# Optimization experiments

Measured on AMD Instinct MI355X. Metric: run time of the kernel, lower is better.

Reference implementation:

```python
import jax, jax.numpy as jnp
import numpy as np

N_NODES = 100000
N_EDGES = 1600000
D_IN = 128
D_OUT = 128


def setup_inputs() -> dict:
    key = jax.random.key(0)
    k = jax.random.split(key, 6)
    x = jax.random.normal(k[0], (N_NODES, D_IN), dtype=jnp.float32)
    edge_src = jax.random.randint(k[1], (N_EDGES,), 0, N_NODES, dtype=jnp.int64)
    edge_dst = jax.random.randint(k[2], (N_EDGES,), 0, N_NODES, dtype=jnp.int64)
    edge_weight = jax.random.uniform(k[3], (N_EDGES,), dtype=jnp.float32)
    # xavier-uniform-ish init for the two projection matrices
    lim = float(np.sqrt(6.0 / (D_IN + D_OUT)))
    W_nbrs = jax.random.uniform(k[4], (D_IN, D_OUT), minval=-lim, maxval=lim, dtype=jnp.float32)
    W_self = jax.random.uniform(k[5], (D_IN, D_OUT), minval=-lim, maxval=lim, dtype=jnp.float32)
    bias = jnp.zeros((D_OUT,), dtype=jnp.float32)
    return {"x": x, "edge_src": edge_src, "edge_dst": edge_dst,
            "edge_weight": edge_weight, "W_nbrs": W_nbrs, "W_self": W_self,
            "bias": bias}


def reference(x, edge_src, edge_dst, edge_weight, W_nbrs, W_self, bias):
    # y = x @ W_nbrs  (dense projection)
    y = x @ W_nbrs                                   # [N, D_OUT]
    # spmm(adj, y): out[i] = sum_{(j->i) in E} w_ij * y[j]
    msgs = edge_weight[:, None] * y[edge_src]        # [E, D_OUT]
    agg = jax.ops.segment_sum(msgs, edge_dst, num_segments=x.shape[0])
    # self transform + bias
    return agg + x @ W_self + bias
```

## Files before the change

kernel.cpp:

```cpp
#include <hip/hip_runtime.h>
#include <hip/hip_bf16.h>

#define D 128

typedef __bf16 bf16x8 __attribute__((ext_vector_type(8)));
typedef unsigned short u16x8 __attribute__((ext_vector_type(8)));
typedef float f32x4 __attribute__((ext_vector_type(4)));

__device__ __forceinline__ unsigned short f2bf(float f) {
    unsigned u = __float_as_uint(f);
    u += 0x7FFFu + ((u >> 16) & 1u);
    return (unsigned short)(u >> 16);
}
__device__ __forceinline__ float bf2f(unsigned u16) {
    return __uint_as_float(u16 << 16);
}

__global__ void k_build_wt(const float* __restrict__ Wn, const float* __restrict__ Ws,
                           unsigned short* __restrict__ WTs,
                           int* __restrict__ cnt, int N) {
    int g = blockIdx.x * blockDim.x + threadIdx.x;
    int c = g >> 7;
    int k = g & 127;
    float v = (c < 128) ? Wn[k * 128 + c] : Ws[k * 128 + (c - 128)];
    WTs[c * 128 + k] = f2bf(v);
    for (int i = g; i < N; i += 32768) cnt[i] = 0;
}

__global__ __launch_bounds__(256) void k_gemm_rank(
    const float* __restrict__ x, const unsigned short* __restrict__ WTs,
    const float* __restrict__ bias, int N,
    unsigned short* __restrict__ y, float* __restrict__ out,
    const int* __restrict__ edst, int E,
    int* __restrict__ cnt, int* __restrict__ rank) {
    int b = blockIdx.x;
    int tid = threadIdx.x;
    if (b & 1) {
        int e0 = (b >> 1) * 1024 + tid;
        #pragma unroll
        for (int k = 0; k < 4; ++k) {
            int e = e0 + k * 256;
            if (e < E) rank[e] = atomicAdd(&cnt[edst[e]], 1);
        }
        return;
    }
    int gb = b >> 1;
    int brow = gb * 64;
    if (brow >= N) return;
    int w = tid >> 6, l = tid & 63;
    int row0 = brow + w * 16;
    int c15 = l & 15;
    int kgrp = l >> 4;
    int arow = row0 + c15;
    bool avalid = (arow < N);
    const float* xr = x + (size_t)arow * D;
    bf16x8 afrag[4];
    #pragma unroll
    for (int ks = 0; ks < 4; ++ks) {
        int k0 = ks * 32 + kgrp * 8;
        float4 a0, a1;
        if (avalid) { a0 = *(const float4*)(xr + k0); a1 = *(const float4*)(xr + k0 + 4); }
        else { a0 = make_float4(0.f, 0.f, 0.f, 0.f); a1 = a0; }
        bf16x8 f;
        f[0] = (__bf16)a0.x; f[1] = (__bf16)a0.y; f[2] = (__bf16)a0.z; f[3] = (__bf16)a0.w;
        f[4] = (__bf16)a1.x; f[5] = (__bf16)a1.y; f[6] = (__bf16)a1.z; f[7] = (__bf16)a1.w;
        afrag[ks] = f;
    }
    int orow = row0 + kgrp * 4;
    const unsigned short* Bbase = WTs + (size_t)c15 * 128 + kgrp * 8;
    f32x4 acc[8];
    #pragma unroll
    for (int nt = 0; nt < 8; ++nt) {
        f32x4 a = {0.f, 0.f, 0.f, 0.f};
        #pragma unroll
        for (int ks = 0; ks < 4; ++ks) {
            const bf16x8* bp = (const bf16x8*)(Bbase + nt * 16 * 128 + ks * 32);
            a = __builtin_amdgcn_mfma_f32_16x16x32_bf16(afrag[ks], *bp, a, 0, 0, 0);
        }
        acc[nt] = a;
    }
    #pragma unroll
    for (int j = 0; j < 4; ++j) {
        int r = orow + j;
        if (r < N) {
            u16x8 f;
            #pragma unroll
            for (int nt = 0; nt < 8; ++nt) f[nt] = f2bf(acc[nt][j]);
            *(u16x8*)(y + (size_t)r * D + c15 * 8) = f;
        }
    }
    #pragma unroll
    for (int nt = 0; nt < 8; ++nt) {
        f32x4 a = {0.f, 0.f, 0.f, 0.f};
        #pragma unroll
        for (int ks = 0; ks < 4; ++ks) {
            const bf16x8* bp = (const bf16x8*)(Bbase + (128 + nt * 16) * 128 + ks * 32);
            a = __builtin_amdgcn_mfma_f32_16x16x32_bf16(afrag[ks], *bp, a, 0, 0, 0);
        }
        acc[nt] = a;
    }
    float bv[8];
    #pragma unroll
    for (int nt = 0; nt < 8; ++nt) bv[nt] = bias[nt * 16 + c15];
    #pragma unroll
    for (int j = 0; j < 4; ++j) {
        int r = orow + j;
        if (r < N) {
            float4 s0 = make_float4(acc[0][j] + bv[0], acc[1][j] + bv[1],
                                    acc[2][j] + bv[2], acc[3][j] + bv[3]);
            float4 s1 = make_float4(acc[4][j] + bv[4], acc[5][j] + bv[5],
                                    acc[6][j] + bv[6], acc[7][j] + bv[7]);
            float4* op = (float4*)(out + (size_t)r * D + c15 * 8);
            op[0] = s0; op[1] = s1;
        }
    }
}

__global__ void k_scanA(const int* __restrict__ cnt, int N,
                        int* __restrict__ ofs, int* __restrict__ bsum) {
    __shared__ int lds[1024];
    int t = threadIdx.x, i = blockIdx.x * 1024 + t;
    int v = (i < N) ? cnt[i] : 0;
    lds[t] = v; __syncthreads();
    for (int d = 1; d < 1024; d <<= 1) {
        int x = (t >= d) ? lds[t - d] : 0; __syncthreads();
        lds[t] += x; __syncthreads();
    }
    if (i < N) ofs[i] = lds[t] - v;
    if (t == 1023) bsum[blockIdx.x] = lds[t];
}

__global__ void k_scanB(int* __restrict__ bsum, int NB) {
    __shared__ int lds[128];
    int t = threadIdx.x;
    int v = (t < NB) ? bsum[t] : 0;
    lds[t] = v; __syncthreads();
    for (int d = 1; d < 128; d <<= 1) {
        int x = (t >= d) ? lds[t - d] : 0; __syncthreads();
        lds[t] += x; __syncthreads();
    }
    if (t < NB) bsum[t] = lds[t] - v;
}

__global__ __launch_bounds__(256) void k_fill(
    const int* __restrict__ src, const int* __restrict__ dst,
    const float* __restrict__ w, const int* __restrict__ rank, int E,
    const int* __restrict__ ofs, const int* __restrict__ bsum,
    uint2* __restrict__ sorted) {
    int e0 = blockIdx.x * 1024 + threadIdx.x;
    #pragma unroll
    for (int k = 0; k < 4; ++k) {
        int e = e0 + k * 256;
        if (e < E) {
            int d = dst[e];
            int pos = ofs[d] + bsum[d >> 10] + rank[e];
            sorted[pos] = make_uint2((unsigned)src[e], __float_as_uint(w[e]));
        }
    }
}

__global__ __launch_bounds__(256) void k_agg(
    const unsigned short* __restrict__ y, const uint2* __restrict__ sorted,
    const int* __restrict__ ofs, const int* __restrict__ bsum,
    const int* __restrict__ cnt, int N,
    float* __restrict__ out) {
    int w = threadIdx.x >> 6, l = threadIdx.x & 63;
    int node = blockIdx.x * 4 + w;
    if (node >= N) return;
    int s = ofs[node] + bsum[node >> 10], n = cnt[node];
    int g = l >> 4, li = l & 15;
    float4 s0, s1;
    if (l < 16) {
        const float4* spf = (const float4*)(out + (size_t)node * D + li * 8);
        s0 = spf[0]; s1 = spf[1];
    }
    const uint2* sp = sorted + s;
    float a0 = 0.f, a1 = 0.f, a2 = 0.f, a3 = 0.f;
    float a4 = 0.f, a5 = 0.f, a6 = 0.f, a7 = 0.f;
    int j = g;
    for (; j + 4 < n; j += 8) {
        uint2 pa = sp[j];
        uint2 pb = sp[j + 4];
        uint4 va = *(const uint4*)(y + (size_t)pa.x * D + li * 8);
        uint4 vb = *(const uint4*)(y + (size_t)pb.x * D + li * 8);
        float wa = __uint_as_float(pa.y), wb = __uint_as_float(pb.y);
        a0 += wa * bf2f(va.x & 0xFFFFu); a1 += wa * bf2f(va.x >> 16);
        a2 += wa * bf2f(va.y & 0xFFFFu); a3 += wa * bf2f(va.y >> 16);
        a4 += wa * bf2f(va.z & 0xFFFFu); a5 += wa * bf2f(va.z >> 16);
        a6 += wa * bf2f(va.w & 0xFFFFu); a7 += wa * bf2f(va.w >> 16);
        a0 += wb * bf2f(vb.x & 0xFFFFu); a1 += wb * bf2f(vb.x >> 16);
        a2 += wb * bf2f(vb.y & 0xFFFFu); a3 += wb * bf2f(vb.y >> 16);
        a4 += wb * bf2f(vb.z & 0xFFFFu); a5 += wb * bf2f(vb.z >> 16);
        a6 += wb * bf2f(vb.w & 0xFFFFu); a7 += wb * bf2f(vb.w >> 16);
    }
    if (j < n) {
        uint2 p = sp[j];
        uint4 v = *(const uint4*)(y + (size_t)p.x * D + li * 8);
        float wt = __uint_as_float(p.y);
        a0 += wt * bf2f(v.x & 0xFFFFu); a1 += wt * bf2f(v.x >> 16);
        a2 += wt * bf2f(v.y & 0xFFFFu); a3 += wt * bf2f(v.y >> 16);
        a4 += wt * bf2f(v.z & 0xFFFFu); a5 += wt * bf2f(v.z >> 16);
        a6 += wt * bf2f(v.w & 0xFFFFu); a7 += wt * bf2f(v.w >> 16);
    }
    a0 += __shfl_xor(a0, 16, 64); a1 += __shfl_xor(a1, 16, 64);
    a2 += __shfl_xor(a2, 16, 64); a3 += __shfl_xor(a3, 16, 64);
    a4 += __shfl_xor(a4, 16, 64); a5 += __shfl_xor(a5, 16, 64);
    a6 += __shfl_xor(a6, 16, 64); a7 += __shfl_xor(a7, 16, 64);
    a0 += __shfl_xor(a0, 32, 64); a1 += __shfl_xor(a1, 32, 64);
    a2 += __shfl_xor(a2, 32, 64); a3 += __shfl_xor(a3, 32, 64);
    a4 += __shfl_xor(a4, 32, 64); a5 += __shfl_xor(a5, 32, 64);
    a6 += __shfl_xor(a6, 32, 64); a7 += __shfl_xor(a7, 32, 64);
    if (l < 16) {
        float* op = out + (size_t)node * D + li;
        op[0]   = a0 + s0.x; op[16]  = a1 + s0.y;
        op[32]  = a2 + s0.z; op[48]  = a3 + s0.w;
        op[64]  = a4 + s1.x; op[80]  = a5 + s1.y;
        op[96]  = a6 + s1.z; op[112] = a7 + s1.w;
    }
}

extern "C" void kernel_launch(void* const* d_in, const int* in_sizes, int n_in,
                              void* d_out, int out_size, void* d_ws, size_t ws_size,
                              hipStream_t stream) {
    const float* x    = (const float*)d_in[0];
    const int*   esrc = (const int*)d_in[1];
    const int*   edst = (const int*)d_in[2];
    const float* ew   = (const float*)d_in[3];
    const float* Wn   = (const float*)d_in[4];
    const float* Wsf  = (const float*)d_in[5];
    const float* bias = (const float*)d_in[6];
    float* out = (float*)d_out;
    int N = in_sizes[0] / D;
    int E = in_sizes[1];

    char* ws = (char*)d_ws;
    size_t off = 0;
    unsigned short* WTs = (unsigned short*)(ws + off); off += 256 * 128 * sizeof(unsigned short);
    unsigned short* yb  = (unsigned short*)(ws + off); off += (size_t)N * D * sizeof(unsigned short);
    off = (off + 255) & ~(size_t)255;
    int* cnt  = (int*)(ws + off); off += (size_t)N * 4; off = (off + 255) & ~(size_t)255;
    int* ofs  = (int*)(ws + off); off += (size_t)N * 4; off = (off + 255) & ~(size_t)255;
    int* bsum = (int*)(ws + off); off += 1024;
    int* rank = (int*)(ws + off); off += (size_t)E * 4; off = (off + 255) & ~(size_t)255;
    uint2* sorted = (uint2*)(ws + off); off += (size_t)E * 8;

    k_build_wt<<<128, 256, 0, stream>>>(Wn, Wsf, WTs, cnt, N);

    int GB = (N + 63) / 64;
    int RB = (E + 1023) / 1024;
    int G2 = (GB > RB ? GB : RB) * 2;
    k_gemm_rank<<<G2, 256, 0, stream>>>(x, WTs, bias, N, yb, out,
                                        edst, E, cnt, rank);

    int NB = (N + 1023) / 1024;
    k_scanA<<<NB, 1024, 0, stream>>>(cnt, N, ofs, bsum);
    k_scanB<<<1, 128, 0, stream>>>(bsum, NB);
    k_fill<<<(E + 1023) / 1024, 256, 0, stream>>>(esrc, edst, ew, rank, E, ofs, bsum, sorted);

    k_agg<<<(N + 3) / 4, 256, 0, stream>>>(yb, sorted, ofs, bsum, cnt, N, out);
}
```

Before: 352.0 us.

## Stage swizzled weight tiles in LDS and double GEMM rows per block

Weights are now written in an XOR-swizzled transposed layout and staged into 32KB of shared memory per GEMM block, one matrix at a time, instead of being read from global/L2 for every MFMA. Each GEMM block now covers 128 rows (two 16-row tiles per wave), so each weight load is reused across more rows. The block interleave is changed to one GEMM block per two rank blocks to match. This cuts repeated global weight traffic but adds LDS usage that lowers occupancy, plus extra barriers.

Result: faster. 300.6 us (-14.6%).

```diff
diff --git a/kernel.cpp b/kernel.cpp
--- a/kernel.cpp
+++ b/kernel.cpp
@@ -20,10 +20,11 @@
                            unsigned short* __restrict__ WTs,
                            int* __restrict__ cnt, int N) {
     int g = blockIdx.x * blockDim.x + threadIdx.x;
-    int c = g >> 7;
-    int k = g & 127;
+    int k = g >> 8;
+    int c = g & 255;
     float v = (c < 128) ? Wn[k * 128 + c] : Ws[k * 128 + (c - 128)];
-    WTs[c * 128 + k] = f2bf(v);
+    int chunk = k >> 3;
+    WTs[c * 128 + (((chunk ^ (c & 15)) << 3) | (k & 7))] = f2bf(v);
     for (int i = g; i < N; i += 32768) cnt[i] = 0;
 }
 
@@ -33,10 +34,12 @@
     unsigned short* __restrict__ y, float* __restrict__ out,
     const int* __restrict__ edst, int E,
     int* __restrict__ cnt, int* __restrict__ rank) {
+    __shared__ unsigned short sm[128 * 128];
     int b = blockIdx.x;
     int tid = threadIdx.x;
-    if (b & 1) {
-        int e0 = (b >> 1) * 1024 + tid;
+    if (b % 3 != 0) {
+        int rb = (b / 3) * 2 + (b % 3) - 1;
+        int e0 = rb * 1024 + tid;
         #pragma unroll
         for (int k = 0; k < 4; ++k) {
             int e = e0 + k * 256;
@@ -44,74 +47,102 @@
         }
         return;
     }
-    int gb = b >> 1;
-    int brow = gb * 64;
+    int gb = b / 3;
+    int brow = gb * 128;
     if (brow >= N) return;
     int w = tid >> 6, l = tid & 63;
-    int row0 = brow + w * 16;
+    int row0 = brow + w * 32;
     int c15 = l & 15;
     int kgrp = l >> 4;
-    int arow = row0 + c15;
-    bool avalid = (arow < N);
-    const float* xr = x + (size_t)arow * D;
-    bf16x8 afrag[4];
-    #pragma unroll
-    for (int ks = 0; ks < 4; ++ks) {
-        int k0 = ks * 32 + kgrp * 8;
-        float4 a0, a1;
-        if (avalid) { a0 = *(const float4*)(xr + k0); a1 = *(const float4*)(xr + k0 + 4); }
-        else { a0 = make_float4(0.f, 0.f, 0.f, 0.f); a1 = a0; }
-        bf16x8 f;
-        f[0] = (__bf16)a0.x; f[1] = (__bf16)a0.y; f[2] = (__bf16)a0.z; f[3] = (__bf16)a0.w;
-        f[4] = (__bf16)a1.x; f[5] = (__bf16)a1.y; f[6] = (__bf16)a1.z; f[7] = (__bf16)a1.w;
-        afrag[ks] = f;
-    }
-    int orow = row0 + kgrp * 4;
-    const unsigned short* Bbase = WTs + (size_t)c15 * 128 + kgrp * 8;
-    f32x4 acc[8];
-    #pragma unroll
-    for (int nt = 0; nt < 8; ++nt) {
-        f32x4 a = {0.f, 0.f, 0.f, 0.f};
+    const uint4* gs = (const uint4*)WTs;
+    uint4* ss = (uint4*)sm;
+    uint4 st[8];
+    #pragma unroll
+    for (int r = 0; r < 8; ++r) st[r] = gs[r * 256 + tid];
+    bf16x8 afrag[2][4];
+    #pragma unroll
+    for (int rt = 0; rt < 2; ++rt) {
+        int arow = row0 + rt * 16 + c15;
+        bool avalid = (arow < N);
+        const float* xr = x + (size_t)arow * D;
         #pragma unroll
         for (int ks = 0; ks < 4; ++ks) {
-            const bf16x8* bp = (const bf16x8*)(Bbase + nt * 16 * 128 + ks * 32);
-            a = __builtin_amdgcn_mfma_f32_16x16x32_bf16(afrag[ks], *bp, a, 0, 0, 0);
-        }
-        acc[nt] = a;
-    }
-    #pragma unroll
-    for (int j = 0; j < 4; ++j) {
-        int r = orow + j;
-        if (r < N) {
-            u16x8 f;
+            int k0 = ks * 32 + kgrp * 8;
+            float4 a0, a1;
+            if (avalid) { a0 = *(const float4*)(xr + k0); a1 = *(const float4*)(xr + k0 + 4); }
+            else { a0 = make_float4(0.f, 0.f, 0.f, 0.f); a1 = a0; }
+            bf16x8 f;
+            f[0] = (__bf16)a0.x; f[1] = (__bf16)a0.y; f[2] = (__bf16)a0.z; f[3] = (__bf16)a0.w;
+            f[4] = (__bf16)a1.x; f[5] = (__bf16)a1.y; f[6] = (__bf16)a1.z; f[7] = (__bf16)a1.w;
+            afrag[rt][ks] = f;
+        }
+    }
+    #pragma unroll
+    for (int r = 0; r < 8; ++r) ss[r * 256 + tid] = st[r];
+    __syncthreads();
+    #pragma unroll
+    for (int rt = 0; rt < 2; ++rt) {
+        f32x4 acc[8];
+        #pragma unroll
+        for (int nt = 0; nt < 8; ++nt) {
+            int c = nt * 16 + c15;
+            f32x4 a = {0.f, 0.f, 0.f, 0.f};
             #pragma unroll
-            for (int nt = 0; nt < 8; ++nt) f[nt] = f2bf(acc[nt][j]);
-            *(u16x8*)(y + (size_t)r * D + c15 * 8) = f;
-        }
-    }
-    #pragma unroll
-    for (int nt = 0; nt < 8; ++nt) {
-        f32x4 a = {0.f, 0.f, 0.f, 0.f};
-        #pragma unroll
-        for (int ks = 0; ks < 4; ++ks) {
-            const bf16x8* bp = (const bf16x8*)(Bbase + (128 + nt * 16) * 128 + ks * 32);
-            a = __builtin_amdgcn_mfma_f32_16x16x32_bf16(afrag[ks], *bp, a, 0, 0, 0);
-        }
-        acc[nt] = a;
-    }
+            for (int ks = 0; ks < 4; ++ks) {
+                int chunk = ks * 4 + kgrp;
+                const bf16x8* bp = (const bf16x8*)(sm + c * 128 + ((chunk ^ c15) << 3));
+                a = __builtin_amdgcn_mfma_f32_16x16x32_bf16(afrag[rt][ks], *bp, a, 0, 0, 0);
+            }
+            acc[nt] = a;
+        }
+        int orow = row0 + rt * 16 + kgrp * 4;
+        #pragma unroll
+        for (int j = 0; j < 4; ++j) {
+            int r = orow + j;
+            if (r < N) {
+                u16x8 f;
+                #pragma unroll
+                for (int nt = 0; nt < 8; ++nt) f[nt] = f2bf(acc[nt][j]);
+                *(u16x8*)(y + (size_t)r * D + c15 * 8) = f;
+            }
+        }
+    }
+    __syncthreads();
+    #pragma unroll
+    for (int r = 0; r < 8; ++r) st[r] = gs[2048 + r * 256 + tid];
+    #pragma unroll
+    for (int r = 0; r < 8; ++r) ss[r * 256 + tid] = st[r];
+    __syncthreads();
     float bv[8];
     #pragma unroll
     for (int nt = 0; nt < 8; ++nt) bv[nt] = bias[nt * 16 + c15];
     #pragma unroll
-    for (int j = 0; j < 4; ++j) {
-        int r = orow + j;
-        if (r < N) {
-            float4 s0 = make_float4(acc[0][j] + bv[0], acc[1][j] + bv[1],
-                                    acc[2][j] + bv[2], acc[3][j] + bv[3]);
-            float4 s1 = make_float4(acc[4][j] + bv[4], acc[5][j] + bv[5],
-                                    acc[6][j] + bv[6], acc[7][j] + bv[7]);
-            float4* op = (float4*)(out + (size_t)r * D + c15 * 8);
-            op[0] = s0; op[1] = s1;
+    for (int rt = 0; rt < 2; ++rt) {
+        f32x4 acc[8];
+        #pragma unroll
+        for (int nt = 0; nt < 8; ++nt) {
+            int c = nt * 16 + c15;
+            f32x4 a = {0.f, 0.f, 0.f, 0.f};
+            #pragma unroll
+            for (int ks = 0; ks < 4; ++ks) {
+                int chunk = ks * 4 + kgrp;
+                const bf16x8* bp = (const bf16x8*)(sm + c * 128 + ((chunk ^ c15) << 3));
+                a = __builtin_amdgcn_mfma_f32_16x16x32_bf16(afrag[rt][ks], *bp, a, 0, 0, 0);
+            }
+            acc[nt] = a;
+        }
+        int orow = row0 + rt * 16 + kgrp * 4;
+        #pragma unroll
+        for (int j = 0; j < 4; ++j) {
+            int r = orow + j;
+            if (r < N) {
+                float4 s0 = make_float4(acc[0][j] + bv[0], acc[1][j] + bv[1],
+                                        acc[2][j] + bv[2], acc[3][j] + bv[3]);
+                float4 s1 = make_float4(acc[4][j] + bv[4], acc[5][j] + bv[5],
+                                        acc[6][j] + bv[6], acc[7][j] + bv[7]);
+                float4* op = (float4*)(out + (size_t)r * D + c15 * 8);
+                op[0] = s0; op[1] = s1;
+            }
         }
     }
 }
@@ -246,11 +277,12 @@
 
     k_build_wt<<<128, 256, 0, stream>>>(Wn, Wsf, WTs, cnt, N);
 
-    int GB = (N + 63) / 64;
+    int GB = (N + 127) / 128;
     int RB = (E + 1023) / 1024;
-    int G2 = (GB > RB ? GB : RB) * 2;
-    k_gemm_rank<<<G2, 256, 0, stream>>>(x, WTs, bias, N, yb, out,
-                                        edst, E, cnt, rank);
+    int RBH = (RB + 1) / 2;
+    int M = (GB > RBH ? GB : RBH);
+    k_gemm_rank<<<M * 3, 256, 0, stream>>>(x, WTs, bias, N, yb, out,
+                                           edst, E, cnt, rank);
 
     int NB = (N + 1023) / 1024;
     k_scanA<<<NB, 1024, 0, stream>>>(cnt, N, ofs, bsum);
```

## Split GEMM across rank and fill phases, stage weights in swizzled LDS

Applied to the files above, without the earlier changes.

Splits the fused GEMM into two kernels. The neighbour projection runs alongside the edge-rank atomics, and the self projection plus bias runs alongside the sorted-edge fill, which replaces the standalone fill kernel. Each GEMM block now stages its 128x128 bf16 weight half in LDS using an XOR-swizzled layout written by the weight-build kernel, and the rank and fill paths use vectorized int4 loads. This aims to balance work between the two phases and cut repeated global weight reads, at the cost of reading x twice and using 32KB of LDS per block, which can reduce occupancy.

New measurement: 296.6 us. -15.7%, faster.

```diff
diff --git a/kernel.cpp b/kernel.cpp
--- a/kernel.cpp
+++ b/kernel.cpp
@@ -20,27 +20,34 @@
                            unsigned short* __restrict__ WTs,
                            int* __restrict__ cnt, int N) {
     int g = blockIdx.x * blockDim.x + threadIdx.x;
-    int c = g >> 7;
-    int k = g & 127;
+    int k = g >> 8;
+    int c = g & 255;
     float v = (c < 128) ? Wn[k * 128 + c] : Ws[k * 128 + (c - 128)];
-    WTs[c * 128 + k] = f2bf(v);
+    int chunk = k >> 3;
+    WTs[c * 128 + (((chunk ^ (c & 15)) << 3) | (k & 7))] = f2bf(v);
     for (int i = g; i < N; i += 32768) cnt[i] = 0;
 }
 
-__global__ __launch_bounds__(256) void k_gemm_rank(
-    const float* __restrict__ x, const unsigned short* __restrict__ WTs,
-    const float* __restrict__ bias, int N,
-    unsigned short* __restrict__ y, float* __restrict__ out,
+__global__ __launch_bounds__(256) void k1_gemm_y_rank(
+    const float* __restrict__ x, const unsigned short* __restrict__ WTs, int N,
+    unsigned short* __restrict__ y,
     const int* __restrict__ edst, int E,
     int* __restrict__ cnt, int* __restrict__ rank) {
+    __shared__ unsigned short sm[128 * 128];
     int b = blockIdx.x;
     int tid = threadIdx.x;
     if (b & 1) {
-        int e0 = (b >> 1) * 1024 + tid;
-        #pragma unroll
-        for (int k = 0; k < 4; ++k) {
-            int e = e0 + k * 256;
-            if (e < E) rank[e] = atomicAdd(&cnt[edst[e]], 1);
+        int e0 = (b >> 1) * 1024 + tid * 4;
+        if (e0 + 3 < E) {
+            int4 d4 = *(const int4*)(edst + e0);
+            int r0 = atomicAdd(&cnt[d4.x], 1);
+            int r1 = atomicAdd(&cnt[d4.y], 1);
+            int r2 = atomicAdd(&cnt[d4.z], 1);
+            int r3 = atomicAdd(&cnt[d4.w], 1);
+            *(int4*)(rank + e0) = make_int4(r0, r1, r2, r3);
+        } else {
+            for (int e = e0; e < E && e < e0 + 4; ++e)
+                rank[e] = atomicAdd(&cnt[edst[e]], 1);
         }
         return;
     }
@@ -51,6 +58,11 @@
     int row0 = brow + w * 16;
     int c15 = l & 15;
     int kgrp = l >> 4;
+    const uint4* gs = (const uint4*)WTs;
+    uint4* ss = (uint4*)sm;
+    uint4 st[8];
+    #pragma unroll
+    for (int r = 0; r < 8; ++r) st[r] = gs[r * 256 + tid];
     int arow = row0 + c15;
     bool avalid = (arow < N);
     const float* xr = x + (size_t)arow * D;
@@ -66,19 +78,23 @@
         f[4] = (__bf16)a1.x; f[5] = (__bf16)a1.y; f[6] = (__bf16)a1.z; f[7] = (__bf16)a1.w;
         afrag[ks] = f;
     }
-    int orow = row0 + kgrp * 4;
-    const unsigned short* Bbase = WTs + (size_t)c15 * 128 + kgrp * 8;
+    #pragma unroll
+    for (int r = 0; r < 8; ++r) ss[r * 256 + tid] = st[r];
+    __syncthreads();
     f32x4 acc[8];
     #pragma unroll
     for (int nt = 0; nt < 8; ++nt) {
+        int c = nt * 16 + c15;
         f32x4 a = {0.f, 0.f, 0.f, 0.f};
         #pragma unroll
         for (int ks = 0; ks < 4; ++ks) {
-            const bf16x8* bp = (const bf16x8*)(Bbase + nt * 16 * 128 + ks * 32);
+            int chunk = ks * 4 + kgrp;
+            const bf16x8* bp = (const bf16x8*)(sm + c * 128 + ((chunk ^ c15) << 3));
             a = __builtin_amdgcn_mfma_f32_16x16x32_bf16(afrag[ks], *bp, a, 0, 0, 0);
         }
         acc[nt] = a;
     }
+    int orow = row0 + kgrp * 4;
     #pragma unroll
     for (int j = 0; j < 4; ++j) {
         int r = orow + j;
@@ -89,12 +105,104 @@
             *(u16x8*)(y + (size_t)r * D + c15 * 8) = f;
         }
     }
+}
+
+__global__ void k_scanA(const int* __restrict__ cnt, int N,
+                        int* __restrict__ ofs, int* __restrict__ bsum) {
+    __shared__ int lds[1024];
+    int t = threadIdx.x, i = blockIdx.x * 1024 + t;
+    int v = (i < N) ? cnt[i] : 0;
+    lds[t] = v; __syncthreads();
+    for (int d = 1; d < 1024; d <<= 1) {
+        int x = (t >= d) ? lds[t - d] : 0; __syncthreads();
+        lds[t] += x; __syncthreads();
+    }
+    if (i < N) ofs[i] = lds[t] - v;
+    if (t == 1023) bsum[blockIdx.x] = lds[t];
+}
+
+__global__ void k_scanB(int* __restrict__ bsum, int NB) {
+    __shared__ int lds[128];
+    int t = threadIdx.x;
+    int v = (t < NB) ? bsum[t] : 0;
+    lds[t] = v; __syncthreads();
+    for (int d = 1; d < 128; d <<= 1) {
+        int x = (t >= d) ? lds[t - d] : 0; __syncthreads();
+        lds[t] += x; __syncthreads();
+    }
+    if (t < NB) bsum[t] = lds[t] - v;
+}
+
+__global__ __launch_bounds__(256) void k2_gemm_self_fill(
+    const float* __restrict__ x, const unsigned short* __restrict__ WTs,
+    const float* __restrict__ bias, int N,
+    float* __restrict__ out,
+    const int* __restrict__ src, const int* __restrict__ dst,
+    const float* __restrict__ ew, const int* __restrict__ rank, int E,
+    const int* __restrict__ ofs, const int* __restrict__ bsum,
+    uint2* __restrict__ sorted) {
+    __shared__ unsigned short sm[128 * 128];
+    int b = blockIdx.x;
+    int tid = threadIdx.x;
+    if (b & 1) {
+        int e0 = (b >> 1) * 1024 + tid * 4;
+        if (e0 + 3 < E) {
+            int4 d4 = *(const int4*)(dst + e0);
+            int4 s4 = *(const int4*)(src + e0);
+            float4 w4 = *(const float4*)(ew + e0);
+            int4 r4 = *(const int4*)(rank + e0);
+            sorted[ofs[d4.x] + bsum[d4.x >> 10] + r4.x] = make_uint2((unsigned)s4.x, __float_as_uint(w4.x));
+            sorted[ofs[d4.y] + bsum[d4.y >> 10] + r4.y] = make_uint2((unsigned)s4.y, __float_as_uint(w4.y));
+            sorted[ofs[d4.z] + bsum[d4.z >> 10] + r4.z] = make_uint2((unsigned)s4.z, __float_as_uint(w4.z));
+            sorted[ofs[d4.w] + bsum[d4.w >> 10] + r4.w] = make_uint2((unsigned)s4.w, __float_as_uint(w4.w));
+        } else {
+            for (int e = e0; e < E && e < e0 + 4; ++e) {
+                int d = dst[e];
+                sorted[ofs[d] + bsum[d >> 10] + rank[e]] =
+                    make_uint2((unsigned)src[e], __float_as_uint(ew[e]));
+            }
+        }
+        return;
+    }
+    int gb = b >> 1;
+    int brow = gb * 64;
+    if (brow >= N) return;
+    int w = tid >> 6, l = tid & 63;
+    int row0 = brow + w * 16;
+    int c15 = l & 15;
+    int kgrp = l >> 4;
+    const uint4* gs = (const uint4*)WTs;
+    uint4* ss = (uint4*)sm;
+    uint4 st[8];
+    #pragma unroll
+    for (int r = 0; r < 8; ++r) st[r] = gs[2048 + r * 256 + tid];
+    int arow = row0 + c15;
+    bool avalid = (arow < N);
+    const float* xr = x + (size_t)arow * D;
+    bf16x8 afrag[4];
+    #pragma unroll
+    for (int ks = 0; ks < 4; ++ks) {
+        int k0 = ks * 32 + kgrp * 8;
+        float4 a0, a1;
+        if (avalid) { a0 = *(const float4*)(xr + k0); a1 = *(const float4*)(xr + k0 + 4); }
+        else { a0 = make_float4(0.f, 0.f, 0.f, 0.f); a1 = a0; }
+        bf16x8 f;
+        f[0] = (__bf16)a0.x; f[1] = (__bf16)a0.y; f[2] = (__bf16)a0.z; f[3] = (__bf16)a0.w;
+        f[4] = (__bf16)a1.x; f[5] = (__bf16)a1.y; f[6] = (__bf16)a1.z; f[7] = (__bf16)a1.w;
+        afrag[ks] = f;
+    }
+    #pragma unroll
+    for (int r = 0; r < 8; ++r) ss[r * 256 + tid] = st[r];
+    __syncthreads();
+    f32x4 acc[8];
     #pragma unroll
     for (int nt = 0; nt < 8; ++nt) {
+        int c = nt * 16 + c15;
         f32x4 a = {0.f, 0.f, 0.f, 0.f};
         #pragma unroll
         for (int ks = 0; ks < 4; ++ks) {
-            const bf16x8* bp = (const bf16x8*)(Bbase + (128 + nt * 16) * 128 + ks * 32);
+            int chunk = ks * 4 + kgrp;
+            const bf16x8* bp = (const bf16x8*)(sm + c * 128 + ((chunk ^ c15) << 3));
             a = __builtin_amdgcn_mfma_f32_16x16x32_bf16(afrag[ks], *bp, a, 0, 0, 0);
         }
         acc[nt] = a;
@@ -102,6 +210,7 @@
     float bv[8];
     #pragma unroll
     for (int nt = 0; nt < 8; ++nt) bv[nt] = bias[nt * 16 + c15];
+    int orow = row0 + kgrp * 4;
     #pragma unroll
     for (int j = 0; j < 4; ++j) {
         int r = orow + j;
@@ -112,49 +221,6 @@
                                     acc[6][j] + bv[6], acc[7][j] + bv[7]);
             float4* op = (float4*)(out + (size_t)r * D + c15 * 8);
             op[0] = s0; op[1] = s1;
-        }
-    }
-}
-
-__global__ void k_scanA(const int* __restrict__ cnt, int N,
-                        int* __restrict__ ofs, int* __restrict__ bsum) {
-    __shared__ int lds[1024];
-    int t = threadIdx.x, i = blockIdx.x * 1024 + t;
-    int v = (i < N) ? cnt[i] : 0;
-    lds[t] = v; __syncthreads();
-    for (int d = 1; d < 1024; d <<= 1) {
-        int x = (t >= d) ? lds[t - d] : 0; __syncthreads();
-        lds[t] += x; __syncthreads();
-    }
-    if (i < N) ofs[i] = lds[t] - v;
-    if (t == 1023) bsum[blockIdx.x] = lds[t];
-}
-
-__global__ void k_scanB(int* __restrict__ bsum, int NB) {
-    __shared__ int lds[128];
-    int t = threadIdx.x;
-    int v = (t < NB) ? bsum[t] : 0;
-    lds[t] = v; __syncthreads();
-    for (int d = 1; d < 128; d <<= 1) {
-        int x = (t >= d) ? lds[t - d] : 0; __syncthreads();
-        lds[t] += x; __syncthreads();
-    }
-    if (t < NB) bsum[t] = lds[t] - v;
-}
-
-__global__ __launch_bounds__(256) void k_fill(
-    const int* __restrict__ src, const int* __restrict__ dst,
-    const float* __restrict__ w, const int* __restrict__ rank, int E,
-    const int* __restrict__ ofs, const int* __restrict__ bsum,
-    uint2* __restrict__ sorted) {
-    int e0 = blockIdx.x * 1024 + threadIdx.x;
-    #pragma unroll
-    for (int k = 0; k < 4; ++k) {
-        int e = e0 + k * 256;
-        if (e < E) {
-            int d = dst[e];
-            int pos = ofs[d] + bsum[d >> 10] + rank[e];
-            sorted[pos] = make_uint2((unsigned)src[e], __float_as_uint(w[e]));
         }
     }
 }
@@ -248,14 +314,16 @@
 
     int GB = (N + 63) / 64;
     int RB = (E + 1023) / 1024;
-    int G2 = (GB > RB ? GB : RB) * 2;
-    k_gemm_rank<<<G2, 256, 0, stream>>>(x, WTs, bias, N, yb, out,
-                                        edst, E, cnt, rank);
+    int M1 = (GB > RB ? GB : RB);
+    k1_gemm_y_rank<<<M1 * 2, 256, 0, stream>>>(x, WTs, N, yb, edst, E, cnt, rank);
 
     int NB = (N + 1023) / 1024;
     k_scanA<<<NB, 1024, 0, stream>>>(cnt, N, ofs, bsum);
     k_scanB<<<1, 128, 0, stream>>>(bsum, NB);
-    k_fill<<<(E + 1023) / 1024, 256, 0, stream>>>(esrc, edst, ew, rank, E, ofs, bsum, sorted);
+
+    k2_gemm_self_fill<<<M1 * 2, 256, 0, stream>>>(x, WTs, bias, N, out,
+                                                  esrc, edst, ew, rank, E,
+                                                  ofs, bsum, sorted);
 
     k_agg<<<(N + 3) / 4, 256, 0, stream>>>(yb, sorted, ofs, bsum, cnt, N, out);
 }
```
